# Optimization experiments

Measured on AMD Instinct MI355X. Metric: run time of the kernel, lower is better.

Reference implementation:

```python
import jax, jax.numpy as jnp
import numpy as np

# GE2E batch structure: N_SPK speakers, M_UTT utterances each (grouped contiguously),
# first half enrollment (-> centroid), second half test.
N_SPK, M_UTT, D = 1024, 32, 512
M_ENR = M_UTT // 2
EPS = 1e-8  # F.cosine_similarity default eps (clamps norms)


def setup_inputs() -> dict:
    key = jax.random.key(0)
    emb = jax.random.normal(key, (N_SPK * M_UTT, D), dtype=jnp.float32)
    labels = jnp.repeat(jnp.arange(N_SPK, dtype=jnp.int64), M_UTT)
    alpha = jnp.asarray(10.0, dtype=jnp.float32)
    beta = jnp.asarray(-5.0, dtype=jnp.float32)
    return {"embeddings": emb, "labels": labels, "alpha": alpha, "beta": beta}


def reference(embeddings, labels, alpha, beta):
    # labels are contiguously grouped: label i occupies rows [i*M_UTT, (i+1)*M_UTT)
    emb = embeddings.reshape(N_SPK, M_UTT, D)
    enroll = emb[:, :M_ENR]          # [N, M_enr, D]
    test = emb[:, M_ENR:]            # [N, M_tst, D]
    centroid = enroll.mean(axis=1)   # [N, D]

    cent_n = centroid / jnp.maximum(
        jnp.linalg.norm(centroid, axis=-1, keepdims=True), EPS)
    test_n = test / jnp.maximum(
        jnp.linalg.norm(test, axis=-1, keepdims=True), EPS)

    # S[i, j, t] = alpha * cos(centroid_i, test_{j,t}) + beta
    S = alpha * jnp.einsum('id,jtd->ijt', cent_n, test_n) + beta
    E = jnp.exp(S)                                   # [N, N, M_tst]

    idx = jnp.arange(N_SPK)
    pos_sum = E[idx, idx].sum(axis=-1)               # diag: own test vs own centroid
    neg_sum = E.sum(axis=(1, 2)) - pos_sum           # all other speakers' test utts

    loss = (jnp.log(neg_sum) - jnp.log(pos_sum)).mean()
    return loss
```

## Files before the change

### kernel.cpp

```cpp
#include <hip/hip_runtime.h>
#include <math.h>

#define N_SPK 1024
#define M_UTT 32
#define M_ENR 16
#define M_TEST 16
#define D 512
#define N_TEST_ROWS (N_SPK * M_TEST)


typedef __attribute__((ext_vector_type(4))) float f32x4;
typedef __attribute__((ext_vector_type(8))) short short8;
typedef __attribute__((ext_vector_type(8))) unsigned short ushort8;

typedef const __attribute__((address_space(1))) void g_void;
typedef __attribute__((address_space(3))) void lds_void;

__device__ __forceinline__ unsigned short f2bf(float f) {
    unsigned int u = __float_as_uint(f);
    u += 0x7FFF + ((u >> 16) & 1);
    return (unsigned short)(u >> 16);
}

__global__ __launch_bounds__(256) void prep_kernel(const float* __restrict__ emb,
                                                   unsigned short* __restrict__ cent,
                                                   unsigned short* __restrict__ test,
                                                   float* __restrict__ g_row,
                                                   float* __restrict__ g_pos) {
    const int b = blockIdx.x;
    const int tid = threadIdx.x;
    const int lane = tid & 63;
    const int wid = tid >> 6;

    if (b < 4) {
        g_row[b * 256 + tid] = 0.f;
        g_pos[b * 256 + tid] = 0.f;
    }

    if (b < N_SPK) {
        const float2* base2 = (const float2*)(emb + (size_t)b * M_UTT * D);
        float a0 = 0.f, a1 = 0.f;
#pragma unroll
        for (int u = 0; u < M_ENR; ++u) {
            const float2 v = base2[u * 256 + tid];
            a0 += v.x; a1 += v.y;
        }
        a0 *= (1.f / 16.f);
        a1 *= (1.f / 16.f);
        float ss = a0 * a0 + a1 * a1;
#pragma unroll
        for (int m = 1; m < 64; m <<= 1) ss += __shfl_xor(ss, m, 64);
        __shared__ float wss[4];
        if (lane == 0) wss[wid] = ss;
        __syncthreads();
        const float tot = wss[0] + wss[1] + wss[2] + wss[3];
        const float inv = 1.f / fmaxf(sqrtf(tot), 1e-8f);
        ushort2 o2;
        o2.x = f2bf(a0 * inv);
        o2.y = f2bf(a1 * inv);
        *(ushort2*)&cent[b * D + 2 * tid] = o2;
    } else {
        const int r = (b - N_SPK) * 4 + wid;
        const int s = r >> 4, t = r & 15;
        const float* row = emb + ((size_t)s * M_UTT + M_ENR + t) * D;
        const f32x4* rv = (const f32x4*)row;
        const f32x4 v0 = rv[lane * 2];
        const f32x4 v1 = rv[lane * 2 + 1];
        float ss = v0[0]*v0[0] + v0[1]*v0[1] + v0[2]*v0[2] + v0[3]*v0[3]
                 + v1[0]*v1[0] + v1[1]*v1[1] + v1[2]*v1[2] + v1[3]*v1[3];
#pragma unroll
        for (int m = 1; m < 64; m <<= 1) ss += __shfl_xor(ss, m, 64);
        const float inv = 1.f / fmaxf(sqrtf(ss), 1e-8f);
        ushort8 o;
        o[0] = f2bf(v0[0] * inv); o[1] = f2bf(v0[1] * inv);
        o[2] = f2bf(v0[2] * inv); o[3] = f2bf(v0[3] * inv);
        o[4] = f2bf(v1[0] * inv); o[5] = f2bf(v1[1] * inv);
        o[6] = f2bf(v1[2] * inv); o[7] = f2bf(v1[3] * inv);
        *(ushort8*)&test[(size_t)r * D + lane * 8] = o;
    }
}

__global__ __launch_bounds__(512) void gemm_kernel(const unsigned short* __restrict__ A,
                                                   const unsigned short* __restrict__ B,
                                                   const float* __restrict__ alpha_p,
                                                   const float* __restrict__ beta_p,
                                                   float* __restrict__ g_row,
                                                   float* __restrict__ g_pos) {
    __shared__ __align__(16) unsigned short AsL[2 * 256 * 64];
    __shared__ __align__(16) unsigned short BsL[2 * 256 * 64];
    __shared__ float rowsum[256];
    __shared__ float possum[256];

    const int tid = threadIdx.x;
    const int lane = tid & 63;
    const int w = tid >> 6;
    const int wr = w >> 2;
    const int wc = w & 3;
    const int l15 = lane & 15;

    const int raw = blockIdx.x;
    const int wg = (raw & 7) * 32 + (raw >> 3);
    const int bi = wg & 3;
    const int bj = wg >> 2;
    const int row0 = bi * 256, col0 = bj * 256;
    const bool has_diag = ((bj >> 4) == bi);

    const int sw8 = 8 * ((lane & 7) ^ (lane >> 3));
    const int hs = ((lane >> 4) * 8) ^ ((lane & 7) << 3);

    const float alpha = *alpha_p;
    const float beta = *beta_p;

#define STAGE_H(OP, BUF, HF, KT)                                               \
    {                                                                          \
        const unsigned short* gb_ = (OP) ? B : A;                              \
        const int r0_ = ((OP) ? col0 : row0) + (HF) * 128;                     \
        _Pragma("unroll") for (int i_ = 0; i_ < 2; ++i_) {                     \
            const int rl_ = i_ * 64 + w * 8 + (lane >> 3);                     \
            unsigned short* lb_ = ((OP) ? BsL : AsL) +                         \
                (BUF) * 16384 + ((HF) * 128 + i_ * 64 + w * 8) * 64;           \
            __builtin_amdgcn_global_load_lds(                                  \
                (g_void*)&gb_[(size_t)(r0_ + rl_) * D + (KT) * 64 + sw8],      \
                (lds_void*)lb_, 16, 0, 0);                                     \
        }                                                                      \
    }

#define LDA8(BUF, MIH)                                                         \
    _Pragma("unroll") for (int j_ = 0; j_ < 4; ++j_) {                         \
        const int row_ = wr * 128 + ((MIH) * 4 + j_) * 16 + l15;               \
        af[j_ * 2]     = *(const short8*)&AsL[(BUF) * 16384 + row_ * 64 + (0 ^ hs)];  \
        af[j_ * 2 + 1] = *(const short8*)&AsL[(BUF) * 16384 + row_ * 64 + (32 ^ hs)]; \
    }
#define LDB4(DST, BUF, NIH)                                                    \
    _Pragma("unroll") for (int n_ = 0; n_ < 2; ++n_) {                         \
        const int row_ = wc * 64 + ((NIH) * 2 + n_) * 16 + l15;                \
        DST[n_ * 2]     = *(const short8*)&BsL[(BUF) * 16384 + row_ * 64 + (0 ^ hs)];  \
        DST[n_ * 2 + 1] = *(const short8*)&BsL[(BUF) * 16384 + row_ * 64 + (32 ^ hs)]; \
    }

#define MM(BF, MIH, NIH)                                                       \
    {                                                                          \
        __builtin_amdgcn_s_setprio(1);                                         \
        _Pragma("unroll") for (int j_ = 0; j_ < 4; ++j_)                       \
            _Pragma("unroll") for (int n_ = 0; n_ < 2; ++n_)                   \
                _Pragma("unroll") for (int k_ = 0; k_ < 2; ++k_)               \
                    acc[(MIH) * 4 + j_][(NIH) * 2 + n_] =                      \
                        __builtin_amdgcn_mfma_f32_16x16x32_bf16(               \
                            BF[n_ * 2 + k_], af[j_ * 2 + k_],                  \
                            acc[(MIH) * 4 + j_][(NIH) * 2 + n_], 0, 0, 0);     \
        __builtin_amdgcn_s_setprio(0);                                         \
    }

#define VM4 asm volatile("s_waitcnt vmcnt(4)" ::: "memory")
#define VM0 asm volatile("s_waitcnt vmcnt(0)" ::: "memory")
#define BAR __builtin_amdgcn_s_barrier()

    f32x4 acc[8][4] = {};
    short8 af[8], bf0[4], bf1[4];

    STAGE_H(0, 0, 0, 0) STAGE_H(0, 0, 1, 0) STAGE_H(1, 0, 0, 0) STAGE_H(1, 0, 1, 0)
    STAGE_H(1, 1, 0, 1) STAGE_H(1, 1, 1, 1)
    if (tid < 256) { rowsum[tid] = 0.f; possum[tid] = 0.f; }
    VM4;
    BAR;

#pragma unroll
    for (int it = 0; it < 4; ++it) {
        LDA8(0, 0) LDB4(bf0, 0, 0)
        STAGE_H(0, 1, 0, 2 * it + 1)
        BAR; MM(bf0, 0, 0) BAR;

        LDB4(bf1, 0, 1)
        STAGE_H(0, 1, 1, 2 * it + 1)
        BAR; MM(bf1, 0, 1) BAR;

        LDA8(0, 1)
        if (it < 3) STAGE_H(1, 0, 0, 2 * it + 2)
        BAR; MM(bf1, 1, 1) BAR;

        if (it < 3) { STAGE_H(1, 0, 1, 2 * it + 2) VM4; } else { VM0; }
        BAR; MM(bf0, 1, 0) BAR;

        LDA8(1, 0) LDB4(bf0, 1, 0)
        if (it < 3) STAGE_H(0, 0, 0, 2 * it + 2)
        BAR; MM(bf0, 0, 0) BAR;

        LDB4(bf1, 1, 1)
        if (it < 3) STAGE_H(0, 0, 1, 2 * it + 2)
        BAR; MM(bf1, 0, 1) BAR;

        LDA8(1, 1)
        if (it < 3) STAGE_H(1, 1, 0, 2 * it + 3)
        BAR; MM(bf1, 1, 1) BAR;

        if (it < 3) { STAGE_H(1, 1, 1, 2 * it + 3) VM4; }
        BAR; MM(bf0, 1, 0) BAR;
    }
#undef STAGE_H
#undef LDA8
#undef LDB4
#undef MM
#undef VM4
#undef VM0
#undef BAR

    const int bcol = col0 + wc * 64;
    const int k4 = (lane >> 4) << 2;
#pragma unroll
    for (int mi = 0; mi < 8; ++mi) {
        const int lspk = wr * 128 + mi * 16 + l15;
        const int gs = row0 + lspk;
        float t = 0.f, p = 0.f;
#pragma unroll
        for (int ni = 0; ni < 4; ++ni) {
#pragma unroll
            for (int r = 0; r < 4; ++r) {
                const float e = __expf(fmaf(alpha, acc[mi][ni][r], beta));
                t += e;
                if (has_diag) {
                    const int gt = bcol + ni * 16 + k4 + r;
                    p += ((gt >> 4) == gs) ? e : 0.f;
                }
            }
        }
        t += __shfl_xor(t, 16, 64);
        t += __shfl_xor(t, 32, 64);
        if (lane < 16) atomicAdd(&rowsum[lspk], t);
        if (has_diag) {
            p += __shfl_xor(p, 16, 64);
            p += __shfl_xor(p, 32, 64);
            if (lane < 16) atomicAdd(&possum[lspk], p);
        }
    }
    __syncthreads();
    if (tid < 256) {
        atomicAdd(&g_row[row0 + tid], rowsum[tid]);
        if (has_diag) atomicAdd(&g_pos[row0 + tid], possum[tid]);
    }
}

__global__ __launch_bounds__(1024) void finalize_kernel(const float* __restrict__ g_row,
                                                        const float* __restrict__ g_pos,
                                                        float* __restrict__ out) {
    __shared__ float wsum[16];
    const int i = threadIdx.x;
    const int lane = i & 63, wid = i >> 6;
    const float pos = g_pos[i];
    const float neg = g_row[i] - pos;
    float v = logf(fmaxf(neg, 1e-30f)) - logf(fmaxf(pos, 1e-30f));
#pragma unroll
    for (int m = 1; m < 64; m <<= 1) v += __shfl_xor(v, m, 64);
    if (lane == 0) wsum[wid] = v;
    __syncthreads();
    if (i < 64) {
        float s = (i < 16) ? wsum[i] : 0.f;
#pragma unroll
        for (int m = 1; m < 16; m <<= 1) s += __shfl_xor(s, m, 64);
        if (i == 0) out[0] = s * (1.f / 1024.f);
    }
}

extern "C" void kernel_launch(void* const* d_in, const int* in_sizes, int n_in,
                              void* d_out, int out_size, void* d_ws, size_t ws_size,
                              hipStream_t stream) {
    const float* emb = (const float*)d_in[0];
    const float* alpha_p = (const float*)d_in[2];
    const float* beta_p = (const float*)d_in[3];

    unsigned short* cent = (unsigned short*)d_ws;
    unsigned short* test = cent + (size_t)N_SPK * D;
    float* g_row = (float*)(test + (size_t)N_TEST_ROWS * D);
    float* g_pos = g_row + N_SPK;

    prep_kernel<<<N_SPK + N_TEST_ROWS / 4, 256, 0, stream>>>(emb, cent, test, g_row, g_pos);

    gemm_kernel<<<256, 512, 0, stream>>>(cent, test, alpha_p, beta_p, g_row, g_pos);

    finalize_kernel<<<1, 1024, 0, stream>>>(g_row, g_pos, (float*)d_out);
}
```

Before: 40.55 us.

## Merge GEMM pipeline phases to halve barrier count per iteration

Restructures the software-pipelined main loop from eight barrier-separated phases to four. Each phase now issues both B-fragment loads and both global-to-LDS stages together, then runs two MFMA blocks between one barrier pair. This removes half of the s_barrier synchronisations and gives the scheduler larger MFMA groups to overlap with memory. In exchange, more fragments stay live in registers at once and loads are interleaved with compute at a coarser grain.

```diff
diff --git a/kernel.cpp b/kernel.cpp
--- a/kernel.cpp
+++ b/kernel.cpp
@@ -166,35 +166,22 @@
 
 #pragma unroll
     for (int it = 0; it < 4; ++it) {
-        LDA8(0, 0) LDB4(bf0, 0, 0)
-        STAGE_H(0, 1, 0, 2 * it + 1)
-        BAR; MM(bf0, 0, 0) BAR;
-
-        LDB4(bf1, 0, 1)
-        STAGE_H(0, 1, 1, 2 * it + 1)
-        BAR; MM(bf1, 0, 1) BAR;
+        LDA8(0, 0) LDB4(bf0, 0, 0) LDB4(bf1, 0, 1)
+        STAGE_H(0, 1, 0, 2 * it + 1) STAGE_H(0, 1, 1, 2 * it + 1)
+        BAR; MM(bf0, 0, 0) MM(bf1, 0, 1) BAR;
 
         LDA8(0, 1)
-        if (it < 3) STAGE_H(1, 0, 0, 2 * it + 2)
-        BAR; MM(bf1, 1, 1) BAR;
-
-        if (it < 3) { STAGE_H(1, 0, 1, 2 * it + 2) VM4; } else { VM0; }
-        BAR; MM(bf0, 1, 0) BAR;
-
-        LDA8(1, 0) LDB4(bf0, 1, 0)
-        if (it < 3) STAGE_H(0, 0, 0, 2 * it + 2)
-        BAR; MM(bf0, 0, 0) BAR;
-
-        LDB4(bf1, 1, 1)
-        if (it < 3) STAGE_H(0, 0, 1, 2 * it + 2)
-        BAR; MM(bf1, 0, 1) BAR;
+        if (it < 3) { STAGE_H(1, 0, 0, 2 * it + 2) STAGE_H(1, 0, 1, 2 * it + 2) VM4; }
+        else { VM0; }
+        BAR; MM(bf1, 1, 1) MM(bf0, 1, 0) BAR;
+
+        LDA8(1, 0) LDB4(bf0, 1, 0) LDB4(bf1, 1, 1)
+        if (it < 3) { STAGE_H(0, 0, 0, 2 * it + 2) STAGE_H(0, 0, 1, 2 * it + 2) }
+        BAR; MM(bf0, 0, 0) MM(bf1, 0, 1) BAR;
 
         LDA8(1, 1)
-        if (it < 3) STAGE_H(1, 1, 0, 2 * it + 3)
-        BAR; MM(bf1, 1, 1) BAR;
-
-        if (it < 3) { STAGE_H(1, 1, 1, 2 * it + 3) VM4; }
-        BAR; MM(bf0, 1, 0) BAR;
+        if (it < 3) { STAGE_H(1, 1, 0, 2 * it + 3) STAGE_H(1, 1, 1, 2 * it + 3) VM4; }
+        BAR; MM(bf1, 1, 1) MM(bf0, 1, 0) BAR;
     }
 #undef STAGE_H
 #undef LDA8
```

New measurement: 40.25 us. No clear change (-0.7%).
